# Kernel optimization log

Hardware: AMD Instinct MI355X
Metric: run time of the kernel (lower is better)

Reference implementation:

```python
import jax, jax.numpy as jnp
import numpy as np
import math

N = 20000      # nodes
E = 150000     # edges
IN = 256       # in_dim
HID = 256      # n_hid / out_dim
T = 4          # num_types
R = 8          # num_relations
H = 8          # n_heads
DK = HID // H  # d_k = 32
L = 2          # n_layers
MAXLEN = 240   # RTE max_len


def _rte_table():
    # fixed sinusoid table from RelTemporalEncoding (requires_grad=False in torch)
    pos = np.arange(MAXLEN, dtype=np.float64)[:, None]
    div = np.exp(np.arange(0, HID, 2, dtype=np.float64) * -(math.log(10000.0) / HID))
    emb = np.zeros((MAXLEN, HID), dtype=np.float64)
    emb[:, 0::2] = np.sin(pos * div) / math.sqrt(HID)
    emb[:, 1::2] = np.cos(pos * div) / math.sqrt(HID)
    return jnp.asarray(emb, dtype=jnp.float32)


def setup_inputs() -> dict:
    key = jax.random.key(0)
    ks = jax.random.split(key, 20)
    node_feature = jax.random.normal(ks[0], (N, IN), jnp.float32)
    node_type = jax.random.randint(ks[1], (N,), 0, T)
    edge_index = jax.random.randint(ks[2], (2, E), 0, N)
    edge_type = jax.random.randint(ks[3], (E,), 0, R)
    edge_time = jax.random.randint(ks[4], (E,), 0, MAXLEN)

    s_in = 1.0 / math.sqrt(IN)
    s_h = 1.0 / math.sqrt(HID)
    s_g = math.sqrt(2.0 / (DK + DK))  # glorot for relation mats

    adapt_W = jax.random.normal(ks[5], (T, IN, HID), jnp.float32) * s_in
    adapt_b = jnp.zeros((T, HID), jnp.float32)
    k_W = jax.random.normal(ks[6], (L, T, HID, HID), jnp.float32) * s_h
    k_b = jnp.zeros((L, T, HID), jnp.float32)
    q_W = jax.random.normal(ks[7], (L, T, HID, HID), jnp.float32) * s_h
    q_b = jnp.zeros((L, T, HID), jnp.float32)
    v_W = jax.random.normal(ks[8], (L, T, HID, HID), jnp.float32) * s_h
    v_b = jnp.zeros((L, T, HID), jnp.float32)
    a_W = jax.random.normal(ks[9], (L, T, HID, HID), jnp.float32) * s_h
    a_b = jnp.zeros((L, T, HID), jnp.float32)
    rel_pri = jnp.ones((L, R, H), jnp.float32)
    rel_att = jax.random.normal(ks[10], (L, R, H, DK, DK), jnp.float32) * s_g
    rel_msg = jax.random.normal(ks[11], (L, R, H, DK, DK), jnp.float32) * s_g
    skip = jnp.ones((L, T), jnp.float32)
    rte_W = jax.random.normal(ks[12], (L, HID, HID), jnp.float32) * s_h
    rte_b = jnp.zeros((L, HID), jnp.float32)
    rte_emb = _rte_table()

    return dict(node_feature=node_feature, node_type=node_type, edge_time=edge_time,
                edge_index=edge_index, edge_type=edge_type,
                adapt_W=adapt_W, adapt_b=adapt_b, k_W=k_W, k_b=k_b, q_W=q_W, q_b=q_b,
                v_W=v_W, v_b=v_b, a_W=a_W, a_b=a_b, rel_pri=rel_pri, rel_att=rel_att,
                rel_msg=rel_msg, skip=skip, rte_W=rte_W, rte_b=rte_b, rte_emb=rte_emb)


def _typed_linear(x, W, b, types):
    # x: [M, din]; W: [T, din, dout]; per-row type-selected linear (T dense GEMMs + select)
    out = jnp.zeros((x.shape[0], W.shape[-1]), x.dtype)
    for t in range(T):
        out = jnp.where((types == t)[:, None], x @ W[t] + b[t], out)
    return out


def _hgt_forward(node_feature, node_type, edge_time, edge_index, edge_type,
                 adapt_W, adapt_b, k_W, k_b, q_W, q_b, v_W, v_b, a_W, a_b,
                 rel_pri, rel_att, rel_msg, skip, rte_W, rte_b, rte_emb):
    # adapt: per-type tanh(Linear) (dropout is identity at p=0)
    x = jnp.tanh(_typed_linear(node_feature, adapt_W, adapt_b, node_type))
    src, tgt = edge_index[0], edge_index[1]   # j (source), i (target)
    st, tt = node_type[src], node_type[tgt]
    sqrt_dk = math.sqrt(DK)
    att = None
    rte = rte_emb[edge_time]                  # [E, HID]
    for l in range(L):
        x_j = x[src] + (rte @ rte_W[l] + rte_b[l])   # RTE added to source repr
        x_i = x[tgt]
        q = _typed_linear(x_i, q_W[l], q_b[l], tt).reshape(E, H, DK)
        k = _typed_linear(x_j, k_W[l], k_b[l], st).reshape(E, H, DK)
        v = _typed_linear(x_j, v_W[l], v_b[l], st).reshape(E, H, DK)
        att_e = jnp.zeros((E, H), x.dtype)
        msg = jnp.zeros((E, H, DK), x.dtype)
        for r in range(R):
            kr = jnp.einsum('ehd,hdk->ehk', k, rel_att[l, r])
            vr = jnp.einsum('ehd,hdk->ehk', v, rel_msg[l, r])
            a = (q * kr).sum(-1) * rel_pri[l, r] / sqrt_dk
            m = edge_type == r
            att_e = jnp.where(m[:, None], a, att_e)
            msg = jnp.where(m[:, None, None], vr, msg)
        # segment softmax over target node ids
        amax = jax.ops.segment_max(att_e, tgt, num_segments=N)
        ex = jnp.exp(att_e - amax[tgt])
        denom = jax.ops.segment_sum(ex, tgt, num_segments=N)
        alpha = ex / denom[tgt]                       # [E, H]
        agg = jax.ops.segment_sum(msg * alpha[:, :, None], tgt, num_segments=N)
        agg = jax.nn.gelu(agg.reshape(N, HID), approximate=False)
        trans = _typed_linear(agg, a_W[l], a_b[l], node_type)
        sk = jax.nn.sigmoid(skip[l])[node_type][:, None]
        x = trans * sk + x * (1.0 - sk)               # no LayerNorm (use_norm=False)
        att = alpha
    return att, x


def reference(node_feature, node_type, edge_time, edge_index, edge_type,
              adapt_W, adapt_b, k_W, k_b, q_W, q_b, v_W, v_b, a_W, a_b,
              rel_pri, rel_att, rel_msg, skip, rte_W, rte_b, rte_emb):
    return _hgt_forward(node_feature, node_type, edge_time, edge_index, edge_type,
                        adapt_W, adapt_b, k_W, k_b, q_W, q_b, v_W, v_b, a_W, a_b,
                        rel_pri, rel_att, rel_msg, skip, rte_W, rte_b, rte_emb)
```

## Files before the change

kernel.cpp:

```cpp
#include <hip/hip_runtime.h>
#include <hip/hip_fp16.h>

#define NN    20000
#define NE    150000
#define HD    256
#define NT    4
#define NR    8
#define NH    8
#define DKq   32
#define NL    2
#define MAXL  240
#define HBLK  256
#define SCB   ((NN + 255)/256)
#define TMAX  632
#define FOLDN 79
#define FOLDC 15
#define INV_SQRT_DK 0.17677669529663687f

typedef _Float16 f16x4 __attribute__((ext_vector_type(4)));
typedef float    f32x4v __attribute__((ext_vector_type(4)));

__global__ __launch_bounds__(256) void k_nhist(const int* __restrict__ ntype, int* __restrict__ nhist)
{
    __shared__ int h[NT];
    const int tid = threadIdx.x, b = blockIdx.x;
    if (tid < NT) h[tid] = 0;
    __syncthreads();
    const int cn = (NN + HBLK-1)/HBLK;
    const int nEnd = min((b+1)*cn, NN);
    for (int i = b*cn + tid; i < nEnd; i += 256) atomicAdd(&h[ntype[i]], 1);
    __syncthreads();
    if (tid < NT) nhist[b*NT + tid] = h[tid];
}
__global__ void k_nscan(const int* __restrict__ nhist, int* __restrict__ noff, int* __restrict__ nbase,
                        int* __restrict__ tlist, int* __restrict__ tcount)
{
    __shared__ int tot[NT];
    const int tid = threadIdx.x;
    if (tid < NT){
        int s = 0;
        for (int b = 0; b < HBLK; b++) s += nhist[b*NT + tid];
        tot[tid] = s;
    }
    __syncthreads();
    if (tid == 0){ noff[0]=0; for (int t=0;t<NT;t++) noff[t+1]=noff[t]+tot[t]; }
    if (tid < NT){
        int base = 0; for (int t=0;t<tid;t++) base += tot[t];
        int run = 0;
        for (int b=0;b<HBLK;b++){ nbase[b*NT+tid] = base + run; run += nhist[b*NT+tid]; }
    }
    __syncthreads();
    if (tid == 0){
        int c = 0;
        for (int t = 0; t < NT; t++){
            const int ntile = (tot[t] + 31) >> 5;
            for (int rt = 0; rt < ntile; rt++) tlist[c++] = (t << 20) | rt;
        }
        *tcount = c;
    }
}
__global__ __launch_bounds__(256) void k_nscatter(const int* __restrict__ ntype,
    const int* __restrict__ nbase, int* __restrict__ nbucket)
{
    __shared__ int cur[NT];
    const int tid = threadIdx.x, b = blockIdx.x;
    if (tid < NT) cur[tid] = nbase[b*NT + tid];
    __syncthreads();
    const int cn = (NN + HBLK-1)/HBLK;
    const int nEnd = min((b+1)*cn, NN);
    for (int i = b*cn + tid; i < nEnd; i += 256)
        nbucket[atomicAdd(&cur[ntype[i]], 1)] = i;
}

__global__ void k_zero_bins(int* __restrict__ cnt){
    int i = blockIdx.x*256 + threadIdx.x;
    if (i < NN) cnt[i] = 0;
}
__global__ void k_csr_hist(const int* __restrict__ ei, int* __restrict__ cnt){
    int e = blockIdx.x*256 + threadIdx.x;
    if (e >= NE) return;
    atomicAdd(&cnt[ei[NE+e]], 1);
}
__global__ __launch_bounds__(256) void k_scan1(const int* __restrict__ cnt,
    int* __restrict__ tgt_off, int* __restrict__ bsum)
{
    __shared__ int sh[256];
    const int t = threadIdx.x, b = blockIdx.x;
    const int i = b*256 + t;
    const int v = (i < NN) ? cnt[i] : 0;
    sh[t] = v;
    __syncthreads();
    #pragma unroll
    for (int d = 1; d < 256; d <<= 1){
        const int u = (t >= d) ? sh[t-d] : 0;
        __syncthreads();
        sh[t] += u;
        __syncthreads();
    }
    if (i < NN) tgt_off[i] = sh[t] - v;
    if (t == 255) bsum[b] = sh[255];
}
__global__ __launch_bounds__(128) void k_scan2(const int* __restrict__ bsum,
    int* __restrict__ bbase, int* __restrict__ tgt_off)
{
    __shared__ int sh[128];
    const int t = threadIdx.x;
    const int v = (t < SCB) ? bsum[t] : 0;
    sh[t] = v;
    __syncthreads();
    #pragma unroll
    for (int d = 1; d < 128; d <<= 1){
        const int u = (t >= d) ? sh[t-d] : 0;
        __syncthreads();
        sh[t] += u;
        __syncthreads();
    }
    if (t < SCB) bbase[t] = sh[t] - v;
    if (t == 0) tgt_off[NN] = NE;
}
__global__ __launch_bounds__(256) void k_scan3(int* __restrict__ tgt_off,
    const int* __restrict__ bbase, int* __restrict__ binCur)
{
    const int i = blockIdx.x*256 + threadIdx.x;
    if (i >= NN) return;
    const int o = tgt_off[i] + bbase[blockIdx.x];
    tgt_off[i] = o;
    binCur[i] = o;
}
__global__ void k_csr_scatter(const int* __restrict__ ei, const int* __restrict__ etype,
    const int* __restrict__ etime, const int* __restrict__ ntype,
    int* __restrict__ binCur, int* __restrict__ src_s, int* __restrict__ combo_s,
    int* __restrict__ eid_s)
{
    int e = blockIdx.x*256 + threadIdx.x;
    if (e >= NE) return;
    const int tgt = ei[NE+e], r = etype[e], src = ei[e];
    const int pos = atomicAdd(&binCur[tgt], 1);
    src_s[pos] = src;
    combo_s[pos] = (etime[e]*NT + ntype[src]) | (r << 12);
    eid_s[pos] = e;
}

__global__ __launch_bounds__(256) void k_w2f16_big(
    const float* __restrict__ adaptW, const float* __restrict__ qW, const float* __restrict__ kW,
    const float* __restrict__ vW, const float* __restrict__ aW, _Float16* __restrict__ out)
{
    const int y = blockIdx.y;
    const float* src; int m;
    if (y < 4){ src = adaptW; m = y; }
    else if (y < 12){ src = qW; m = y-4; }
    else if (y < 20){ src = kW; m = y-12; }
    else if (y < 28){ src = vW; m = y-20; }
    else { src = aW; m = y-28; }
    const float* ip = src + (size_t)m*65536;
    _Float16* op = out + (size_t)y*65536;
    const int tid4 = blockIdx.x*256 + threadIdx.x;
    const int k4 = tid4 >> 8, c = tid4 & 255;
    f16x4 hv;
    #pragma unroll
    for (int j = 0; j < 4; j++)
        hv[j] = (_Float16)ip[(size_t)(((k4*4 + j) << 8) + c)];
    *reinterpret_cast<f16x4*>(&op[(size_t)tid4 * 4]) = hv;
}
__global__ __launch_bounds__(256) void k_w2f16_rel(
    const float* __restrict__ attW, const float* __restrict__ msgW, _Float16* __restrict__ out)
{
    const int y = blockIdx.y;
    const float* ip = (y < 128) ? (attW + (size_t)y*1024) : (msgW + (size_t)(y-128)*1024);
    _Float16* op = out + (size_t)y*1024;
    const int tid4 = threadIdx.x;
    const int k4 = tid4 >> 5, c = tid4 & 31;
    f16x4 hv;
    #pragma unroll
    for (int j = 0; j < 4; j++)
        hv[j] = (_Float16)ip[(size_t)(((k4*4 + j) << 5) + c)];
    *reinterpret_cast<f16x4*>(&op[(size_t)tid4 * 4]) = hv;
}

__global__ __launch_bounds__(256) void k_typed_fused(
    const float* __restrict__ inF, const _Float16* __restrict__ inH,
    const _Float16* __restrict__ Wa, const float* __restrict__ ba, void* __restrict__ oa,
    const _Float16* __restrict__ Wq, const float* __restrict__ bq, void* __restrict__ oq,
    const _Float16* __restrict__ Wk, const float* __restrict__ bk, void* __restrict__ ok_,
    const _Float16* __restrict__ Wv, const float* __restrict__ bv, void* __restrict__ ov,
    const int* __restrict__ nbucket, const int* __restrict__ noff,
    const int* __restrict__ tlist, const int* __restrict__ tcount,
    int mode, int ohmask, const float* __restrict__ skipv, const float* __restrict__ xold)
{
    if ((int)blockIdx.x >= *tcount) return;
    const int ent = tlist[blockIdx.x];
    const int t = ent >> 20, rowTile = ent & 0xFFFFF;
    const int start = noff[t], cnt = noff[t+1] - start;

    const int tid = threadIdx.x;
    const int w = tid >> 6, lane = tid & 63;
    const int lrow = lane & 15, lgrp = lane >> 4;

    __shared__ _Float16 Al[32][260];
    __shared__ int nid[32];

    if (tid < 32){
        const int gr = rowTile*32 + tid;
        nid[tid] = (gr < cnt) ? nbucket[start + gr] : -1;
    }
    __syncthreads();

    {
        const int r = tid >> 3;
        const int arow = nid[r];
        if (inH){
            const _Float16* ap = (arow >= 0) ? (inH + (size_t)arow*HD) : nullptr;
            #pragma unroll
            for (int j = 0; j < 8; j++){
                const int f4 = (tid & 7) + j*8;
                f16x4 hv = {0,0,0,0};
                if (ap) hv = *reinterpret_cast<const f16x4*>(ap + f4*4);
                *reinterpret_cast<f16x4*>(&Al[r][f4*4]) = hv;
            }
        } else {
            const float* ap = (arow >= 0) ? (inF + (size_t)arow*HD) : nullptr;
            #pragma unroll
            for (int j = 0; j < 8; j++){
                const int f4 = (tid & 7) + j*8;
                float4 v = make_float4(0.f,0.f,0.f,0.f);
                if (ap) v = *reinterpret_cast<const float4*>(ap + f4*4);
                f16x4 hv;
                hv[0]=(_Float16)v.x; hv[1]=(_Float16)v.y; hv[2]=(_Float16)v.z; hv[3]=(_Float16)v.w;
                *reinterpret_cast<f16x4*>(&Al[r][f4*4]) = hv;
            }
        }
    }
    __syncthreads();

    float sk = 0.f;
    if (mode == 2) sk = 1.f/(1.f + __expf(-skipv[t]));

    const bool chain = (Wq != nullptr);

    auto proc = [&](const _Float16* Wb, const float* bb, void* out, int oh, int md, bool cw){
        const _Float16* W = Wb + (size_t)t*HD*HD;
        const float* bias = bb + (size_t)t*HD;
        f32x4v acc[4][2];
        #pragma unroll
        for (int cs = 0; cs < 4; cs++){
            acc[cs][0] = (f32x4v){0.f,0.f,0.f,0.f};
            acc[cs][1] = (f32x4v){0.f,0.f,0.f,0.f};
        }
        #pragma unroll 4
        for (int kc = 0; kc < 16; kc++){
            f16x4 bf[4];
            #pragma unroll
            for (int cs = 0; cs < 4; cs++)
                bf[cs] = *reinterpret_cast<const f16x4*>(
                    &W[(size_t)((kc*4 + lgrp)*HD + w*64 + cs*16 + lrow)*4]);
            const f16x4 af0 = *reinterpret_cast<const f16x4*>(&Al[lrow][kc*16 + lgrp*4]);
            const f16x4 af1 = *reinterpret_cast<const f16x4*>(&Al[16 + lrow][kc*16 + lgrp*4]);
            #pragma unroll
            for (int cs = 0; cs < 4; cs++){
                acc[cs][0] = __builtin_amdgcn_mfma_f32_16x16x16f16(af0, bf[cs], acc[cs][0], 0,0,0);
                acc[cs][1] = __builtin_amdgcn_mfma_f32_16x16x16f16(af1, bf[cs], acc[cs][1], 0,0,0);
            }
        }
        if (cw) __syncthreads();
        #pragma unroll
        for (int cs = 0; cs < 4; cs++){
            const int col = w*64 + cs*16 + lrow;
            const float bcol = bias[col];
            #pragma unroll
            for (int rt = 0; rt < 2; rt++){
                #pragma unroll
                for (int i = 0; i < 4; i++){
                    const int lr = rt*16 + lgrp*4 + i;
                    const int gr = rowTile*32 + lr;
                    if (gr >= cnt) continue;
                    const int node = nid[lr];
                    float v = acc[cs][rt][i] + bcol;
                    if (md == 1) v = tanhf(v);
                    else if (md == 2){
                        const float xo = xold[(size_t)node*HD + col];
                        v = v*sk + xo*(1.f - sk);
                    }
                    if (oh) ((_Float16*)out)[(size_t)node*HD + col] = (_Float16)v;
                    else    ((float*)out)[(size_t)node*HD + col] = v;
                    if (cw) Al[lr][col] = (_Float16)v;
                }
            }
        }
        if (cw) __syncthreads();
    };

    proc(Wa, ba, oa, ohmask & 1, mode, chain);
    if (chain){
        proc(Wq, bq, oq, (ohmask >> 1) & 1, 0, false);
        proc(Wk, bk, ok_, (ohmask >> 2) & 1, 0, false);
        proc(Wv, bv, ov, (ohmask >> 3) & 1, 0, false);
    }
}

__global__ __launch_bounds__(256) void k_row_gemm(
    const float* __restrict__ A, const float* __restrict__ W, const float* __restrict__ bias,
    float* __restrict__ C)
{
    const int row = blockIdx.x, d = threadIdx.x;
    __shared__ float ar[HD];
    ar[d] = A[(size_t)row*HD + d];
    __syncthreads();
    float acc = bias[d];
    #pragma unroll 8
    for (int k=0;k<HD;k++) acc = fmaf(ar[k], W[(size_t)k*HD + d], acc);
    C[(size_t)row*HD + d] = acc;
}
__global__ __launch_bounds__(256) void k_row_gemm2(
    const float* __restrict__ A, const float* __restrict__ kWb, const float* __restrict__ vWb,
    _Float16* __restrict__ Kc, _Float16* __restrict__ Vc)
{
    const int row = blockIdx.x, ty = blockIdx.y, d = threadIdx.x;
    const float* W = ((blockIdx.z == 0) ? kWb : vWb) + (size_t)ty*HD*HD;
    _Float16* C = (blockIdx.z == 0) ? Kc : Vc;
    __shared__ float ar[HD];
    ar[d] = A[(size_t)row*HD + d];
    __syncthreads();
    float acc = 0.f;
    #pragma unroll 8
    for (int k=0;k<HD;k++) acc = fmaf(ar[k], W[(size_t)k*HD + d], acc);
    C[(size_t)row*(NT*HD) + ty*HD + d] = (_Float16)acc;
}

__global__ __launch_bounds__(256) void k_fold_mfma(
    const _Float16* __restrict__ IN, const _Float16* __restrict__ MATF,
    _Float16* __restrict__ OUT, int M, int nbx)
{
    const int r = blockIdx.y;
    const int lane = threadIdx.x & 63, w = threadIdx.x >> 6;
    const int lrow = lane & 15, lgrp = lane >> 4;
    f16x4 b[NH][2][2];
    const _Float16* Mr = MATF + (size_t)r*NH*1024;
    #pragma unroll
    for (int h = 0; h < NH; h++)
      #pragma unroll
      for (int kb = 0; kb < 2; kb++)
        #pragma unroll
        for (int hf = 0; hf < 2; hf++)
            b[h][kb][hf] = *reinterpret_cast<const f16x4*>(
                &Mr[(size_t)h*1024 + (size_t)(((kb*4 + lgrp)*32) + hf*16 + lrow)*4]);
    const int ntiles = M >> 4;
    for (int t = (int)blockIdx.x*4 + w; t < ntiles; t += nbx*4){
        const int row0 = t*16;
        const _Float16* inrow = IN + (size_t)(row0 + lrow)*HD;
        f16x4 a[NH][2];
        #pragma unroll
        for (int h = 0; h < NH; h++)
          #pragma unroll
          for (int kb = 0; kb < 2; kb++)
              a[h][kb] = *reinterpret_cast<const f16x4*>(&inrow[h*32 + kb*16 + lgrp*4]);
        #pragma unroll
        for (int h = 0; h < NH; h++){
          #pragma unroll
          for (int hf = 0; hf < 2; hf++){
              f32x4v acc = {0.f,0.f,0.f,0.f};
              acc = __builtin_amdgcn_mfma_f32_16x16x16f16(a[h][0], b[h][0][hf], acc, 0,0,0);
              acc = __builtin_amdgcn_mfma_f32_16x16x16f16(a[h][1], b[h][1][hf], acc, 0,0,0);
              #pragma unroll
              for (int i = 0; i < 4; i++){
                  const int rr = lgrp*4 + i;
                  OUT[((size_t)(row0+rr)*NR + r)*HD + h*32 + hf*16 + lrow] = (_Float16)acc[i];
              }
          }
        }
    }
}

__global__ __launch_bounds__(256) void k_scoresm(
    const _Float16* __restrict__ q0, const _Float16* __restrict__ kA, const _Float16* __restrict__ KcA,
    const float* __restrict__ relP,
    const int* __restrict__ tgt_off, const int* __restrict__ src_s, const int* __restrict__ combo_s,
    const int* __restrict__ eid_s,
    float* __restrict__ s_arr, float* __restrict__ out_att, int store_s)
{
    const int n = blockIdx.x*4 + (threadIdx.x >> 6);
    if (n >= NN) return;
    const int lane = threadIdx.x & 63;
    const int h = lane >> 3, c4 = (lane & 7) << 2;
    const int col = h*32 + c4;
    const int e0 = tgt_off[n], e1 = tgt_off[n+1];
    if (e0 == e1) return;

    const f16x4 qh = *reinterpret_cast<const f16x4*>(&q0[(size_t)n*HD + col]);
    const float q0v = (float)qh[0], q1v = (float)qh[1], q2v = (float)qh[2], q3v = (float)qh[3];
    float m = -INFINITY;
    for (int j = e0; j < e1; j++){
        const int src = src_s[j];
        const int cw  = combo_s[j];
        const int r = cw >> 12, combo = cw & 0xFFF;
        const f16x4 ka = *reinterpret_cast<const f16x4*>(&kA[((size_t)src*NR + r)*HD + col]);
        const f16x4 kc = *reinterpret_cast<const f16x4*>(&KcA[((size_t)combo*NR + r)*HD + col]);
        float s = q0v*((float)ka[0]+(float)kc[0])
                + q1v*((float)ka[1]+(float)kc[1])
                + q2v*((float)ka[2]+(float)kc[2])
                + q3v*((float)ka[3]+(float)kc[3]);
        s += __shfl_xor(s, 1); s += __shfl_xor(s, 2); s += __shfl_xor(s, 4);
        s *= relP[r*NH + h] * INV_SQRT_DK;
        if ((lane & 7) == 0) s_arr[(size_t)j*NH + h] = s;
        m = fmaxf(m, s);
    }
    if ((lane & 7) == 0){
        float l = 0.f;
        for (int j = e0; j < e1; j++){
            const float e = __expf(s_arr[(size_t)j*NH + h] - m);
            s_arr[(size_t)j*NH + h] = e;
            l += e;
        }
        const float inv = 1.f / l;
        for (int j = e0; j < e1; j++){
            const float a = s_arr[(size_t)j*NH + h] * inv;
            s_arr[(size_t)j*NH + h] = a;
            if (store_s) out_att[(size_t)eid_s[j]*NH + h] = a;
        }
    }
}

__global__ __launch_bounds__(256) void k_agg(
    const _Float16* __restrict__ vM, const _Float16* __restrict__ VcM,
    const float* __restrict__ alpha,
    const int* __restrict__ tgt_off, const int* __restrict__ src_s, const int* __restrict__ combo_s,
    _Float16* __restrict__ agg)
{
    const int n = blockIdx.x*4 + (threadIdx.x >> 6);
    if (n >= NN) return;
    const int lane = threadIdx.x & 63;
    const int h = lane >> 3, c4 = (lane & 7) << 2;
    const int col = h*32 + c4;
    const int e0 = tgt_off[n], e1 = tgt_off[n+1];
    float a0=0.f, a1=0.f, a2=0.f, a3=0.f;
    for (int j = e0; j < e1; j++){
        const int src = src_s[j];
        const int cw  = combo_s[j];
        const int r = cw >> 12, combo = cw & 0xFFF;
        const float al = alpha[(size_t)j*NH + h];
        const f16x4 vm = *reinterpret_cast<const f16x4*>(&vM[((size_t)src*NR + r)*HD + col]);
        const f16x4 vc = *reinterpret_cast<const f16x4*>(&VcM[((size_t)combo*NR + r)*HD + col]);
        a0 = fmaf(al, (float)vm[0] + (float)vc[0], a0);
        a1 = fmaf(al, (float)vm[1] + (float)vc[1], a1);
        a2 = fmaf(al, (float)vm[2] + (float)vc[2], a2);
        a3 = fmaf(al, (float)vm[3] + (float)vc[3], a3);
    }
    f16x4 o;
    o[0] = (_Float16)(0.5f*a0*(1.f + erff(a0*0.70710678118654752f)));
    o[1] = (_Float16)(0.5f*a1*(1.f + erff(a1*0.70710678118654752f)));
    o[2] = (_Float16)(0.5f*a2*(1.f + erff(a2*0.70710678118654752f)));
    o[3] = (_Float16)(0.5f*a3*(1.f + erff(a3*0.70710678118654752f)));
    *reinterpret_cast<f16x4*>(&agg[(size_t)n*HD + col]) = o;
}

extern "C" void kernel_launch(void* const* d_in, const int* in_sizes, int n_in,
                              void* d_out, int out_size, void* d_ws, size_t ws_size,
                              hipStream_t stream)
{
    const float* node_feature = (const float*)d_in[0];
    const int*   node_type    = (const int*)d_in[1];
    const int*   edge_time    = (const int*)d_in[2];
    const int*   edge_index   = (const int*)d_in[3];
    const int*   edge_type    = (const int*)d_in[4];
    const float* adapt_W = (const float*)d_in[5];
    const float* adapt_b = (const float*)d_in[6];
    const float* k_W = (const float*)d_in[7];
    const float* k_b = (const float*)d_in[8];
    const float* q_W = (const float*)d_in[9];
    const float* q_b = (const float*)d_in[10];
    const float* v_W = (const float*)d_in[11];
    const float* v_b = (const float*)d_in[12];
    const float* a_W = (const float*)d_in[13];
    const float* a_b = (const float*)d_in[14];
    const float* rel_pri = (const float*)d_in[15];
    const float* rel_att = (const float*)d_in[16];
    const float* rel_msg = (const float*)d_in[17];
    const float* skip  = (const float*)d_in[18];
    const float* rte_W = (const float*)d_in[19];
    const float* rte_b = (const float*)d_in[20];
    const float* rte_emb = (const float*)d_in[21];

    char* wp = (char*)d_ws;
    auto alloc_f = [&](size_t n)->float*{ float* p=(float*)wp; wp += n*sizeof(float); return p; };
    auto alloc_i = [&](size_t n)->int*  { int*   p=(int*)wp;   wp += n*sizeof(int);   return p; };
    auto alloc_h = [&](size_t n)->_Float16*{ _Float16* p=(_Float16*)wp; wp += n*sizeof(_Float16); return p; };
    float* xA    = alloc_f((size_t)NN*HD);
    float* xB    = alloc_f((size_t)NN*HD);
    _Float16* q0h = alloc_h((size_t)NN*HD);
    _Float16* k0h = alloc_h((size_t)NN*HD);
    _Float16* v0h = alloc_h((size_t)NN*HD);
    _Float16* aggh= alloc_h((size_t)NN*HD);
    float* s_arr = alloc_f((size_t)NE*NH);
    float* rteP  = alloc_f((size_t)MAXL*HD);
    _Float16* Kch = alloc_h((size_t)MAXL*NT*HD);
    _Float16* Vch = alloc_h((size_t)MAXL*NT*HD);
    _Float16* kavm = alloc_h((size_t)NN*NR*HD);
    _Float16* kcaA0 = alloc_h((size_t)MAXL*NT*NR*HD);
    _Float16* kcaA1 = alloc_h((size_t)MAXL*NT*NR*HD);
    _Float16* kcaM0 = alloc_h((size_t)MAXL*NT*NR*HD);
    _Float16* kcaM1 = alloc_h((size_t)MAXL*NT*NR*HD);
    _Float16* wF   = alloc_h((size_t)36*65536);
    _Float16* relF = alloc_h((size_t)256*1024);
    int* nbucket = alloc_i(NN);
    int* nhist   = alloc_i(HBLK*NT);
    int* nbase   = alloc_i(HBLK*NT);
    int* noff    = alloc_i(8);
    int* tlist   = alloc_i(TMAX);
    int* tcount  = alloc_i(8);
    int* cnt     = alloc_i(NN);
    int* bsum    = alloc_i(SCB);
    int* bbase   = alloc_i(SCB);
    int* binCur  = alloc_i(NN);
    int* tgt_off = alloc_i(NN+1);
    int* src_s   = alloc_i(NE);
    int* combo_s = alloc_i(NE);
    int* eid_s   = alloc_i(NE);

    const _Float16* adaptF = wF;
    const _Float16* qF = wF + (size_t)4*65536;
    const _Float16* kF = wF + (size_t)12*65536;
    const _Float16* vF = wF + (size_t)20*65536;
    const _Float16* aF = wF + (size_t)28*65536;
    const _Float16* relAF = relF;
    const _Float16* relMF = relF + (size_t)128*1024;

    float* out_att = (float*)d_out;
    float* out_x   = (float*)d_out + (size_t)NE*NH;

    const dim3 gFoldN(FOLDN, NR);
    const dim3 gFoldC(FOLDC, NR);
    const int gE256 = (NE + 255)/256;
    const int gEg = (NN + 3)/4;

    k_w2f16_big<<<dim3(64,36),256,0,stream>>>(adapt_W, q_W, k_W, v_W, a_W, wF);
    k_w2f16_rel<<<dim3(1,256),256,0,stream>>>(rel_att, rel_msg, relF);

    k_nhist<<<HBLK,256,0,stream>>>(node_type, nhist);
    k_nscan<<<1,64,0,stream>>>(nhist, noff, nbase, tlist, tcount);
    k_nscatter<<<HBLK,256,0,stream>>>(node_type, nbase, nbucket);

    k_zero_bins<<<SCB,256,0,stream>>>(cnt);
    k_csr_hist<<<gE256,256,0,stream>>>(edge_index, cnt);
    k_scan1<<<SCB,256,0,stream>>>(cnt, tgt_off, bsum);
    k_scan2<<<1,128,0,stream>>>(bsum, bbase, tgt_off);
    k_scan3<<<SCB,256,0,stream>>>(tgt_off, bbase, binCur);
    k_csr_scatter<<<gE256,256,0,stream>>>(edge_index, edge_type, edge_time, node_type,
                                          binCur, src_s, combo_s, eid_s);

    {
        k_row_gemm<<<MAXL,256,0,stream>>>(rte_emb, rte_W, rte_b, rteP);
        k_row_gemm2<<<dim3(MAXL,NT,2),256,0,stream>>>(rteP, k_W, v_W, Kch, Vch);
        k_fold_mfma<<<gFoldC,256,0,stream>>>(Kch, relAF, kcaA0, MAXL*NT, FOLDC);
        k_fold_mfma<<<gFoldC,256,0,stream>>>(Vch, relMF, kcaM0, MAXL*NT, FOLDC);
        k_row_gemm<<<MAXL,256,0,stream>>>(rte_emb, rte_W + (size_t)HD*HD, rte_b + HD, rteP);
        k_row_gemm2<<<dim3(MAXL,NT,2),256,0,stream>>>(rteP, k_W + (size_t)NT*HD*HD,
                                                      v_W + (size_t)NT*HD*HD, Kch, Vch);
        k_fold_mfma<<<gFoldC,256,0,stream>>>(Kch, relAF + (size_t)NR*NH*1024, kcaA1, MAXL*NT, FOLDC);
        k_fold_mfma<<<gFoldC,256,0,stream>>>(Vch, relMF + (size_t)NR*NH*1024, kcaM1, MAXL*NT, FOLDC);
    }

    k_typed_fused<<<TMAX,256,0,stream>>>(node_feature, nullptr,
                                         adaptF, adapt_b, xA,
                                         qF, q_b, q0h,
                                         kF, k_b, k0h,
                                         vF, v_b, v0h,
                                         nbucket, noff, tlist, tcount,
                                         1, 14, nullptr, nullptr);

    for (int l = 0; l < NL; l++){
        const _Float16* rAF = relAF + (size_t)l*NR*NH*1024;
        const _Float16* rMF = relMF + (size_t)l*NR*NH*1024;
        const _Float16* kcaA = (l == 0) ? kcaA0 : kcaA1;
        const _Float16* kcaM = (l == 0) ? kcaM0 : kcaM1;
        const int store_s = (l == NL-1) ? 1 : 0;
        k_fold_mfma<<<gFoldN,256,0,stream>>>(k0h, rAF, kavm, NN, FOLDN);
        k_scoresm<<<gEg,256,0,stream>>>(q0h, kavm, kcaA, rel_pri + (size_t)l*NR*NH,
                                        tgt_off, src_s, combo_s, eid_s,
                                        s_arr, out_att, store_s);
        k_fold_mfma<<<gFoldN,256,0,stream>>>(v0h, rMF, kavm, NN, FOLDN);
        k_agg<<<gEg,256,0,stream>>>(kavm, kcaM, s_arr, tgt_off, src_s, combo_s, aggh);
        if (l == 0){
            k_typed_fused<<<TMAX,256,0,stream>>>(nullptr, aggh,
                                                 aF, a_b, xB,
                                                 qF + (size_t)NT*HD*HD, q_b + (size_t)NT*HD, q0h,
                                                 kF + (size_t)NT*HD*HD, k_b + (size_t)NT*HD, k0h,
                                                 vF + (size_t)NT*HD*HD, v_b + (size_t)NT*HD, v0h,
                                                 nbucket, noff, tlist, tcount,
                                                 2, 14, skip, xA);
        } else {
            k_typed_fused<<<TMAX,256,0,stream>>>(nullptr, aggh,
                                                 aF + (size_t)NT*HD*HD, a_b + (size_t)NT*HD, out_x,
                                                 nullptr, nullptr, nullptr,
                                                 nullptr, nullptr, nullptr,
                                                 nullptr, nullptr, nullptr,
                                                 nbucket, noff, tlist, tcount,
                                                 2, 0, skip + NT, xB);
        }
    }
}
```

Before: 601.2 us.

## Split fused typed GEMM chain into separate x and parallel QKV kernels

The fused kernel that computed the typed linear output and then chained Q, K and V projections serially per block is split into two kernels. One computes x, and a second launch uses a 3-wide y grid so Q, K and V tiles run in parallel blocks. This raises parallelism beyond the roughly 632 blocks available before. The intermediate x is now stored in fp16 instead of fp32, which halves its traffic but adds an extra write and re-read of x, an extra launch, and some precision loss in the residual path.

```diff
diff --git a/kernel.cpp b/kernel.cpp
--- a/kernel.cpp
+++ b/kernel.cpp
@@ -177,15 +177,12 @@
     *reinterpret_cast<f16x4*>(&op[(size_t)tid4 * 4]) = hv;
 }
 
-__global__ __launch_bounds__(256) void k_typed_fused(
+__global__ __launch_bounds__(256) void k_x(
     const float* __restrict__ inF, const _Float16* __restrict__ inH,
-    const _Float16* __restrict__ Wa, const float* __restrict__ ba, void* __restrict__ oa,
-    const _Float16* __restrict__ Wq, const float* __restrict__ bq, void* __restrict__ oq,
-    const _Float16* __restrict__ Wk, const float* __restrict__ bk, void* __restrict__ ok_,
-    const _Float16* __restrict__ Wv, const float* __restrict__ bv, void* __restrict__ ov,
+    const _Float16* __restrict__ Wb, const float* __restrict__ bb, void* __restrict__ out,
     const int* __restrict__ nbucket, const int* __restrict__ noff,
     const int* __restrict__ tlist, const int* __restrict__ tcount,
-    int mode, int ohmask, const float* __restrict__ skipv, const float* __restrict__ xold)
+    int mode, int oh, const float* __restrict__ skipv, const _Float16* __restrict__ xoldH)
 {
     if ((int)blockIdx.x >= *tcount) return;
     const int ent = tlist[blockIdx.x];
@@ -204,7 +201,6 @@
         nid[tid] = (gr < cnt) ? nbucket[start + gr] : -1;
     }
     __syncthreads();
-
     {
         const int r = tid >> 3;
         const int arow = nid[r];
@@ -235,65 +231,135 @@
     float sk = 0.f;
     if (mode == 2) sk = 1.f/(1.f + __expf(-skipv[t]));
 
-    const bool chain = (Wq != nullptr);
-
-    auto proc = [&](const _Float16* Wb, const float* bb, void* out, int oh, int md, bool cw){
-        const _Float16* W = Wb + (size_t)t*HD*HD;
-        const float* bias = bb + (size_t)t*HD;
-        f32x4v acc[4][2];
+    const _Float16* W = Wb + (size_t)t*HD*HD;
+    const float* bias = bb + (size_t)t*HD;
+    f32x4v acc[4][2];
+    #pragma unroll
+    for (int cs = 0; cs < 4; cs++){
+        acc[cs][0] = (f32x4v){0.f,0.f,0.f,0.f};
+        acc[cs][1] = (f32x4v){0.f,0.f,0.f,0.f};
+    }
+    #pragma unroll 4
+    for (int kc = 0; kc < 16; kc++){
+        f16x4 bf[4];
+        #pragma unroll
+        for (int cs = 0; cs < 4; cs++)
+            bf[cs] = *reinterpret_cast<const f16x4*>(
+                &W[(size_t)((kc*4 + lgrp)*HD + w*64 + cs*16 + lrow)*4]);
+        const f16x4 af0 = *reinterpret_cast<const f16x4*>(&Al[lrow][kc*16 + lgrp*4]);
+        const f16x4 af1 = *reinterpret_cast<const f16x4*>(&Al[16 + lrow][kc*16 + lgrp*4]);
         #pragma unroll
         for (int cs = 0; cs < 4; cs++){
-            acc[cs][0] = (f32x4v){0.f,0.f,0.f,0.f};
-            acc[cs][1] = (f32x4v){0.f,0.f,0.f,0.f};
-        }
-        #pragma unroll 4
-        for (int kc = 0; kc < 16; kc++){
-            f16x4 bf[4];
+            acc[cs][0] = __builtin_amdgcn_mfma_f32_16x16x16f16(af0, bf[cs], acc[cs][0], 0,0,0);
+            acc[cs][1] = __builtin_amdgcn_mfma_f32_16x16x16f16(af1, bf[cs], acc[cs][1], 0,0,0);
+        }
+    }
+    #pragma unroll
+    for (int cs = 0; cs < 4; cs++){
+        const int col = w*64 + cs*16 + lrow;
+        const float bcol = bias[col];
+        #pragma unroll
+        for (int rt = 0; rt < 2; rt++){
             #pragma unroll
-            for (int cs = 0; cs < 4; cs++)
-                bf[cs] = *reinterpret_cast<const f16x4*>(
-                    &W[(size_t)((kc*4 + lgrp)*HD + w*64 + cs*16 + lrow)*4]);
-            const f16x4 af0 = *reinterpret_cast<const f16x4*>(&Al[lrow][kc*16 + lgrp*4]);
-            const f16x4 af1 = *reinterpret_cast<const f16x4*>(&Al[16 + lrow][kc*16 + lgrp*4]);
+            for (int i = 0; i < 4; i++){
+                const int lr = rt*16 + lgrp*4 + i;
+                const int gr = rowTile*32 + lr;
+                if (gr >= cnt) continue;
+                const int node = nid[lr];
+                float v = acc[cs][rt][i] + bcol;
+                if (mode == 1) v = tanhf(v);
+                else if (mode == 2){
+                    const float xo = (float)xoldH[(size_t)node*HD + col];
+                    v = v*sk + xo*(1.f - sk);
+                }
+                if (oh) ((_Float16*)out)[(size_t)node*HD + col] = (_Float16)v;
+                else    ((float*)out)[(size_t)node*HD + col] = v;
+            }
+        }
+    }
+}
+
+__global__ __launch_bounds__(256) void k_qkv(
+    const _Float16* __restrict__ xh,
+    const _Float16* __restrict__ Wq, const float* __restrict__ bq, _Float16* __restrict__ oq,
+    const _Float16* __restrict__ Wk, const float* __restrict__ bk, _Float16* __restrict__ okk,
+    const _Float16* __restrict__ Wv, const float* __restrict__ bv, _Float16* __restrict__ ov,
+    const int* __restrict__ nbucket, const int* __restrict__ noff,
+    const int* __restrict__ tlist, const int* __restrict__ tcount)
+{
+    if ((int)blockIdx.x >= *tcount) return;
+    const int ent = tlist[blockIdx.x];
+    const int t = ent >> 20, rowTile = ent & 0xFFFFF;
+    const int start = noff[t], cnt = noff[t+1] - start;
+    const int sel = blockIdx.y;
+    const _Float16* Wb = (sel==0 ? Wq : (sel==1 ? Wk : Wv));
+    const float* bb = (sel==0 ? bq : (sel==1 ? bk : bv));
+    _Float16* out = (sel==0 ? oq : (sel==1 ? okk : ov));
+
+    const int tid = threadIdx.x;
+    const int w = tid >> 6, lane = tid & 63;
+    const int lrow = lane & 15, lgrp = lane >> 4;
+
+    __shared__ _Float16 Al[32][260];
+    __shared__ int nid[32];
+
+    if (tid < 32){
+        const int gr = rowTile*32 + tid;
+        nid[tid] = (gr < cnt) ? nbucket[start + gr] : -1;
+    }
+    __syncthreads();
+    {
+        const int r = tid >> 3;
+        const int arow = nid[r];
+        const _Float16* ap = (arow >= 0) ? (xh + (size_t)arow*HD) : nullptr;
+        #pragma unroll
+        for (int j = 0; j < 8; j++){
+            const int f4 = (tid & 7) + j*8;
+            f16x4 hv = {0,0,0,0};
+            if (ap) hv = *reinterpret_cast<const f16x4*>(ap + f4*4);
+            *reinterpret_cast<f16x4*>(&Al[r][f4*4]) = hv;
+        }
+    }
+    __syncthreads();
+
+    const _Float16* W = Wb + (size_t)t*HD*HD;
+    const float* bias = bb + (size_t)t*HD;
+    f32x4v acc[4][2];
+    #pragma unroll
+    for (int cs = 0; cs < 4; cs++){
+        acc[cs][0] = (f32x4v){0.f,0.f,0.f,0.f};
+        acc[cs][1] = (f32x4v){0.f,0.f,0.f,0.f};
+    }
+    #pragma unroll 4
+    for (int kc = 0; kc < 16; kc++){
+        f16x4 bf[4];
+        #pragma unroll
+        for (int cs = 0; cs < 4; cs++)
+            bf[cs] = *reinterpret_cast<const f16x4*>(
+                &W[(size_t)((kc*4 + lgrp)*HD + w*64 + cs*16 + lrow)*4]);
+        const f16x4 af0 = *reinterpret_cast<const f16x4*>(&Al[lrow][kc*16 + lgrp*4]);
+        const f16x4 af1 = *reinterpret_cast<const f16x4*>(&Al[16 + lrow][kc*16 + lgrp*4]);
+        #pragma unroll
+        for (int cs = 0; cs < 4; cs++){
+            acc[cs][0] = __builtin_amdgcn_mfma_f32_16x16x16f16(af0, bf[cs], acc[cs][0], 0,0,0);
+            acc[cs][1] = __builtin_amdgcn_mfma_f32_16x16x16f16(af1, bf[cs], acc[cs][1], 0,0,0);
+        }
+    }
+    #pragma unroll
+    for (int cs = 0; cs < 4; cs++){
+        const int col = w*64 + cs*16 + lrow;
+        const float bcol = bias[col];
+        #pragma unroll
+        for (int rt = 0; rt < 2; rt++){
             #pragma unroll
-            for (int cs = 0; cs < 4; cs++){
-                acc[cs][0] = __builtin_amdgcn_mfma_f32_16x16x16f16(af0, bf[cs], acc[cs][0], 0,0,0);
-                acc[cs][1] = __builtin_amdgcn_mfma_f32_16x16x16f16(af1, bf[cs], acc[cs][1], 0,0,0);
+            for (int i = 0; i < 4; i++){
+                const int lr = rt*16 + lgrp*4 + i;
+                const int gr = rowTile*32 + lr;
+                if (gr >= cnt) continue;
+                const int node = nid[lr];
+                out[(size_t)node*HD + col] = (_Float16)(acc[cs][rt][i] + bcol);
             }
         }
-        if (cw) __syncthreads();
-        #pragma unroll
-        for (int cs = 0; cs < 4; cs++){
-            const int col = w*64 + cs*16 + lrow;
-            const float bcol = bias[col];
-            #pragma unroll
-            for (int rt = 0; rt < 2; rt++){
-                #pragma unroll
-                for (int i = 0; i < 4; i++){
-                    const int lr = rt*16 + lgrp*4 + i;
-                    const int gr = rowTile*32 + lr;
-                    if (gr >= cnt) continue;
-                    const int node = nid[lr];
-                    float v = acc[cs][rt][i] + bcol;
-                    if (md == 1) v = tanhf(v);
-                    else if (md == 2){
-                        const float xo = xold[(size_t)node*HD + col];
-                        v = v*sk + xo*(1.f - sk);
-                    }
-                    if (oh) ((_Float16*)out)[(size_t)node*HD + col] = (_Float16)v;
-                    else    ((float*)out)[(size_t)node*HD + col] = v;
-                    if (cw) Al[lr][col] = (_Float16)v;
-                }
-            }
-        }
-        if (cw) __syncthreads();
-    };
-
-    proc(Wa, ba, oa, ohmask & 1, mode, chain);
-    if (chain){
-        proc(Wq, bq, oq, (ohmask >> 1) & 1, 0, false);
-        proc(Wk, bk, ok_, (ohmask >> 2) & 1, 0, false);
-        proc(Wv, bv, ov, (ohmask >> 3) & 1, 0, false);
     }
 }
 
@@ -483,8 +549,8 @@
     auto alloc_f = [&](size_t n)->float*{ float* p=(float*)wp; wp += n*sizeof(float); return p; };
     auto alloc_i = [&](size_t n)->int*  { int*   p=(int*)wp;   wp += n*sizeof(int);   return p; };
     auto alloc_h = [&](size_t n)->_Float16*{ _Float16* p=(_Float16*)wp; wp += n*sizeof(_Float16); return p; };
-    float* xA    = alloc_f((size_t)NN*HD);
-    float* xB    = alloc_f((size_t)NN*HD);
+    _Float16* xh0 = alloc_h((size_t)NN*HD);
+    _Float16* xh1 = alloc_h((size_t)NN*HD);
     _Float16* q0h = alloc_h((size_t)NN*HD);
     _Float16* k0h = alloc_h((size_t)NN*HD);
     _Float16* v0h = alloc_h((size_t)NN*HD);
@@ -528,6 +594,7 @@
 
     const dim3 gFoldN(FOLDN, NR);
     const dim3 gFoldC(FOLDC, NR);
+    const dim3 gQKV(TMAX, 3);
     const int gE256 = (NE + 255)/256;
     const int gEg = (NN + 3)/4;
 
@@ -558,13 +625,10 @@
         k_fold_mfma<<<gFoldC,256,0,stream>>>(Vch, relMF + (size_t)NR*NH*1024, kcaM1, MAXL*NT, FOLDC);
     }
 
-    k_typed_fused<<<TMAX,256,0,stream>>>(node_feature, nullptr,
-                                         adaptF, adapt_b, xA,
-                                         qF, q_b, q0h,
-                                         kF, k_b, k0h,
-                                         vF, v_b, v0h,
-                                         nbucket, noff, tlist, tcount,
-                                         1, 14, nullptr, nullptr);
+    k_x<<<TMAX,256,0,stream>>>(node_feature, nullptr, adaptF, adapt_b, xh0,
+                               nbucket, noff, tlist, tcount, 1, 1, nullptr, nullptr);
+    k_qkv<<<gQKV,256,0,stream>>>(xh0, qF, q_b, q0h, kF, k_b, k0h, vF, v_b, v0h,
+                                 nbucket, noff, tlist, tcount);
 
     for (int l = 0; l < NL; l++){
         const _Float16* rAF = relAF + (size_t)l*NR*NH*1024;
@@ -579,21 +643,15 @@
         k_fold_mfma<<<gFoldN,256,0,stream>>>(v0h, rMF, kavm, NN, FOLDN);
         k_agg<<<gEg,256,0,stream>>>(kavm, kcaM, s_arr, tgt_off, src_s, combo_s, aggh);
         if (l == 0){
-            k_typed_fused<<<TMAX,256,0,stream>>>(nullptr, aggh,
-                                                 aF, a_b, xB,
-                                                 qF + (size_t)NT*HD*HD, q_b + (size_t)NT*HD, q0h,
-                                                 kF + (size_t)NT*HD*HD, k_b + (size_t)NT*HD, k0h,
-                                                 vF + (size_t)NT*HD*HD, v_b + (size_t)NT*HD, v0h,
-                                                 nbucket, noff, tlist, tcount,
-                                                 2, 14, skip, xA);
+            k_x<<<TMAX,256,0,stream>>>(nullptr, aggh, aF, a_b, xh1,
+                                       nbucket, noff, tlist, tcount, 2, 1, skip, xh0);
+            k_qkv<<<gQKV,256,0,stream>>>(xh1, qF + (size_t)NT*HD*HD, q_b + (size_t)NT*HD, q0h,
+                                         kF + (size_t)NT*HD*HD, k_b + (size_t)NT*HD, k0h,
+                                         vF + (size_t)NT*HD*HD, v_b + (size_t)NT*HD, v0h,
+                                         nbucket, noff, tlist, tcount);
         } else {
-            k_typed_fused<<<TMAX,256,0,stream>>>(nullptr, aggh,
-                                                 aF + (size_t)NT*HD*HD, a_b + (size_t)NT*HD, out_x,
-                                                 nullptr, nullptr, nullptr,
-                                                 nullptr, nullptr, nullptr,
-                                                 nullptr, nullptr, nullptr,
-                                                 nbucket, noff, tlist, tcount,
-                                                 2, 0, skip + NT, xB);
-        }
-    }
-}
+            k_x<<<TMAX,256,0,stream>>>(nullptr, aggh, aF + (size_t)NT*HD*HD, a_b + (size_t)NT*HD,
+                                       out_x, nbucket, noff, tlist, tcount, 2, 0, skip + NT, xh1);
+        }
+    }
+}
```

Result: no change. 602.9 us (+0.3%).
